# Optimization experiments

Hardware: AMD Instinct MI355X
Metric: run time of the kernel (lower is better)

The kernel has to match this reference:

```python
import jax, jax.numpy as jnp
import numpy as np

N = 100000      # nodes
E = 3200000     # edges (avg degree 32)
F_IN = 512      # num_features
H = 256         # hidden
C = 64          # num_classes
K = 20          # APPNP propagation steps
ALPHA = 0.1     # teleport probability


def setup_inputs() -> dict:
    key = jax.random.key(0)
    k0, k1, k2, k3 = jax.random.split(key, 4)
    x = jax.random.normal(k0, (N, F_IN), dtype=jnp.float32)
    edge_index = jax.random.randint(k1, (2, E), 0, N, dtype=jnp.int64)
    W1 = jax.random.normal(k2, (F_IN, H), dtype=jnp.float32) / np.sqrt(F_IN).astype(np.float32)
    b1 = jnp.zeros((H,), jnp.float32)
    W2 = jax.random.normal(k3, (H, C), dtype=jnp.float32) / np.sqrt(H).astype(np.float32)
    b2 = jnpp = jnp.zeros((C,), jnp.float32)
    return {"x": x, "edge_index": edge_index, "W1": W1, "b1": b1, "W2": W2, "b2": b2}


def reference(x, edge_index, W1, b1, W2, b2):
    n = x.shape[0]
    # MLP encoder (dropout is identity in eval mode)
    h = jax.nn.relu(x @ W1 + b1) @ W2 + b2            # [N, C]

    # gcn_norm with added self-loops (PyG APPNP default)
    self_loop = jnp.arange(n, dtype=edge_index.dtype)
    src = jnp.concatenate([edge_index[0], self_loop])  # message sources
    dst = jnp.concatenate([edge_index[1], self_loop])  # aggregation targets
    deg = jax.ops.segment_sum(jnp.ones_like(dst, jnp.float32), dst, num_segments=n)
    deg_inv_sqrt = jnp.where(deg > 0, jax.lax.rsqrt(deg), 0.0)
    norm = (deg_inv_sqrt[src] * deg_inv_sqrt[dst])[:, None]  # [E+N, 1]

    def prop_step(_, z):
        msg = z[src] * norm                               # gather + scale
        agg = jax.ops.segment_sum(msg, dst, num_segments=n)  # scatter-add
        return (1.0 - ALPHA) * agg + ALPHA * h            # teleport mix

    z = jax.lax.fori_loop(0, K, prop_step, h)
    return jax.nn.log_softmax(z, axis=1)
```

## Files before the change

### kernel.cpp

```cpp
#include <hip/hip_runtime.h>
#include <hip/hip_bf16.h>
#include <math.h>

#define NN 100000
#define EE 3200000
#define FIN 512
#define HID 256
#define CLS 64
#define KST 20

typedef __attribute__((ext_vector_type(8))) short bf16x8;
typedef __attribute__((ext_vector_type(4))) float f32x4;

__device__ __forceinline__ short f2bf(float f) {
    union { __hip_bfloat16 b; short s; } u;
    u.b = __float2bfloat16(f);
    return u.s;
}
__device__ __forceinline__ float bf2f(__hip_bfloat16 b) { return __bfloat162float(b); }


__global__ void zero_kernel(int* __restrict__ degcnt, int* __restrict__ cursor) {
    int i = blockIdx.x * 256 + threadIdx.x;
    if (i < NN) { degcnt[i] = 0; cursor[i] = 0; }
}

__global__ void count_kernel(const int* __restrict__ edst, int* __restrict__ degcnt) {
    int e = blockIdx.x * 256 + threadIdx.x;
    if (e < EE) atomicAdd(&degcnt[edst[e]], 1);
}

__global__ __launch_bounds__(1024) void scan1_kernel(const int* __restrict__ degcnt,
                                                     int* __restrict__ tmp,
                                                     int* __restrict__ bsum) {
    __shared__ int s[1024];
    int t = threadIdx.x;
    int i = blockIdx.x * 1024 + t;
    int v = (i < NN) ? degcnt[i] : 0;
    s[t] = v;
    __syncthreads();
    for (int off = 1; off < 1024; off <<= 1) {
        int xv = (t >= off) ? s[t - off] : 0;
        __syncthreads();
        s[t] += xv;
        __syncthreads();
    }
    if (i < NN) tmp[i] = s[t] - v;
    if (t == 1023) bsum[blockIdx.x] = s[1023];
}

__global__ void scan2_kernel(const int* __restrict__ bsum, int* __restrict__ boff, int nb) {
    if (blockIdx.x == 0 && threadIdx.x == 0) {
        int run = 0;
        for (int b = 0; b < nb; ++b) { boff[b] = run; run += bsum[b]; }
    }
}

__global__ void finalize_kernel(const int* __restrict__ tmp, const int* __restrict__ boff,
                                const int* __restrict__ degcnt,
                                int* __restrict__ rowptr, float* __restrict__ dis) {
    int i = blockIdx.x * 256 + threadIdx.x;
    if (i < NN) {
        rowptr[i] = tmp[i] + boff[i >> 10];
        dis[i] = rsqrtf((float)(degcnt[i] + 1));
        if (i == 0) rowptr[NN] = EE;
    }
}

__global__ void fill_kernel(const int* __restrict__ esrc, const int* __restrict__ edst,
                            const int* __restrict__ rowptr, int* __restrict__ cursor,
                            int* __restrict__ csrc) {
    int e = blockIdx.x * 256 + threadIdx.x;
    if (e < EE) {
        int d = edst[e];
        int pos = atomicAdd(&cursor[d], 1);
        csrc[rowptr[d] + pos] = esrc[e];
    }
}


__global__ void w1t_kernel(const float* __restrict__ W1, __hip_bfloat16* __restrict__ W1Tt) {
    const int c = threadIdx.x;
    const int kg = blockIdx.x;
    bf16x8 o;
#pragma unroll
    for (int j = 0; j < 8; ++j) o[j] = f2bf(W1[(size_t)(kg * 8 + j) * HID + c]);
    size_t dst = ((size_t)((c >> 4) * 16 + (kg >> 2))) * 512 + (c & 15) * 32 + (kg & 3) * 8;
    *(bf16x8*)((short*)W1Tt + dst) = o;
}

__global__ void w2t_kernel(const float* __restrict__ W2, __hip_bfloat16* __restrict__ W2Tt) {
    const int c = threadIdx.x;
    const int kg = blockIdx.x;
    bf16x8 o;
#pragma unroll
    for (int j = 0; j < 8; ++j) o[j] = f2bf(W2[(size_t)(kg * 8 + j) * CLS + c]);
    size_t dst = ((size_t)((c >> 4) * 8 + (kg >> 2))) * 512 + (c & 15) * 32 + (kg & 3) * 8;
    *(bf16x8*)((short*)W2Tt + dst) = o;
}

__device__ __forceinline__ bf16x8 load_a8(const float* p) {
    const float4 f0 = *(const float4*)p;
    const float4 f1 = *(const float4*)(p + 4);
    bf16x8 r;
    r[0] = f2bf(f0.x); r[1] = f2bf(f0.y); r[2] = f2bf(f0.z); r[3] = f2bf(f0.w);
    r[4] = f2bf(f1.x); r[5] = f2bf(f1.y); r[6] = f2bf(f1.z); r[7] = f2bf(f1.w);
    return r;
}

__global__ __launch_bounds__(256, 2) void mlp_kernel(const float* __restrict__ x,
                                                     const __hip_bfloat16* __restrict__ W1Tt,
                                                     const float* __restrict__ b1,
                                                     const __hip_bfloat16* __restrict__ W2Tt,
                                                     const float* __restrict__ b2,
                                                     const float* __restrict__ dis,
                                                     __hip_bfloat16* __restrict__ hb,
                                                     __hip_bfloat16* __restrict__ y0) {
    __shared__ __align__(16) char Tlds[64 * 512];

    const int t = threadIdx.x;
    const int w = t >> 6;
    const int lane = t & 63;
    const int lg = lane >> 4;
    const int li = lane & 15;
    const int loff = li * 32 + lg * 8;
    const int r0 = blockIdx.x * 64;

    const short* W1s = (const short*)W1Tt;
    const short* W2s = (const short*)W2Tt;

    const float* xrow[4];
#pragma unroll
    for (int mf = 0; mf < 4; ++mf) {
        int r = r0 + mf * 16 + li;
        xrow[mf] = x + (size_t)((r < NN) ? r : (NN - 1)) * FIN;
    }

    f32x4 acc1[4][4];
#pragma unroll
    for (int mf = 0; mf < 4; ++mf)
#pragma unroll
        for (int nf = 0; nf < 4; ++nf)
#pragma unroll
            for (int r = 0; r < 4; ++r) acc1[mf][nf][r] = 0.f;

#pragma unroll
    for (int kt = 0; kt < 16; ++kt) {
        bf16x8 bfw[4];
#pragma unroll
        for (int nf = 0; nf < 4; ++nf)
            bfw[nf] = *(const bf16x8*)(W1s + ((size_t)((w * 4 + nf) * 16 + kt)) * 512 + loff);
#pragma unroll
        for (int mf = 0; mf < 4; ++mf) {
            bf16x8 af = load_a8(xrow[mf] + kt * 32 + lg * 8);
#pragma unroll
            for (int nf = 0; nf < 4; ++nf)
                acc1[mf][nf] = __builtin_amdgcn_mfma_f32_16x16x32_bf16(
                    af, bfw[nf], acc1[mf][nf], 0, 0, 0);
        }
    }

#pragma unroll
    for (int nf = 0; nf < 4; ++nf) {
        const float bv = b1[w * 64 + nf * 16 + li];
        const int col = w * 64 + nf * 16 + li;
#pragma unroll
        for (int mf = 0; mf < 4; ++mf) {
#pragma unroll
            for (int r = 0; r < 4; ++r) {
                int row = mf * 16 + lg * 4 + r;
                float tv = fmaxf(acc1[mf][nf][r] + bv, 0.f);
                int byte = row * 512 + ((col * 2) ^ ((row & 7) << 4));
                *(short*)(Tlds + byte) = f2bf(tv);
            }
        }
    }
    __syncthreads();

    f32x4 acc2[4];
#pragma unroll
    for (int nf = 0; nf < 4; ++nf)
#pragma unroll
        for (int r = 0; r < 4; ++r) acc2[nf][r] = 0.f;

#pragma unroll
    for (int kt2 = 0; kt2 < 8; ++kt2) {
        int row = w * 16 + li;
        int kb = (kt2 * 32 + lg * 8) * 2;
        bf16x8 at = *(const bf16x8*)(Tlds + row * 512 + (kb ^ ((row & 7) << 4)));
#pragma unroll
        for (int nf = 0; nf < 4; ++nf) {
            bf16x8 bw = *(const bf16x8*)(W2s + ((size_t)(nf * 8 + kt2)) * 512 + loff);
            acc2[nf] = __builtin_amdgcn_mfma_f32_16x16x32_bf16(at, bw, acc2[nf], 0, 0, 0);
        }
    }

#pragma unroll
    for (int r = 0; r < 4; ++r) {
        int row = r0 + w * 16 + lg * 4 + r;
        if (row < NN) {
            const float dv = dis[row];
#pragma unroll
            for (int nf = 0; nf < 4; ++nf) {
                float hv = acc2[nf][r] + b2[nf * 16 + li];
                size_t o = (size_t)row * CLS + nf * 16 + li;
                hb[o] = __float2bfloat16(hv);
                y0[o] = __float2bfloat16(hv * dv);
            }
        }
    }
}

template <int LAST>
__global__ __launch_bounds__(256) void prop_kernel(const __hip_bfloat16* __restrict__ yin,
                                                   const __hip_bfloat16* __restrict__ hb,
                                                   const float* __restrict__ dis,
                                                   const int* __restrict__ rowptr,
                                                   const int* __restrict__ csrc,
                                                   __hip_bfloat16* __restrict__ yout,
                                                   float* __restrict__ zout) {
    const int node = blockIdx.x * 4 + (threadIdx.x >> 6);
    const int lane = threadIdx.x & 63;

    int p = __builtin_amdgcn_readfirstlane(rowptr[node]);
    const int e = __builtin_amdgcn_readfirstlane(rowptr[node + 1]);

    const __hip_bfloat16* Y = yin + lane;

    float a0 = bf2f(Y[(size_t)node << 6]);
    float a1 = 0.f, a2 = 0.f, a3 = 0.f;

    for (; p + 16 <= e; p += 16) {
        const int4 i0 = *(const int4*)(csrc + p);
        const int4 i1 = *(const int4*)(csrc + p + 4);
        const int4 i2 = *(const int4*)(csrc + p + 8);
        const int4 i3 = *(const int4*)(csrc + p + 12);
        float v0 = bf2f(Y[(size_t)i0.x << 6]);
        float v1 = bf2f(Y[(size_t)i0.y << 6]);
        float v2 = bf2f(Y[(size_t)i0.z << 6]);
        float v3 = bf2f(Y[(size_t)i0.w << 6]);
        float v4 = bf2f(Y[(size_t)i1.x << 6]);
        float v5 = bf2f(Y[(size_t)i1.y << 6]);
        float v6 = bf2f(Y[(size_t)i1.z << 6]);
        float v7 = bf2f(Y[(size_t)i1.w << 6]);
        float v8 = bf2f(Y[(size_t)i2.x << 6]);
        float v9 = bf2f(Y[(size_t)i2.y << 6]);
        float va = bf2f(Y[(size_t)i2.z << 6]);
        float vb = bf2f(Y[(size_t)i2.w << 6]);
        float vc = bf2f(Y[(size_t)i3.x << 6]);
        float vd = bf2f(Y[(size_t)i3.y << 6]);
        float ve = bf2f(Y[(size_t)i3.z << 6]);
        float vf = bf2f(Y[(size_t)i3.w << 6]);
        a0 += (v0 + v1) + (v2 + v3);
        a1 += (v4 + v5) + (v6 + v7);
        a2 += (v8 + v9) + (va + vb);
        a3 += (vc + vd) + (ve + vf);
    }
    for (; p + 4 <= e; p += 4) {
        const int4 i0 = *(const int4*)(csrc + p);
        float v0 = bf2f(Y[(size_t)i0.x << 6]);
        float v1 = bf2f(Y[(size_t)i0.y << 6]);
        float v2 = bf2f(Y[(size_t)i0.z << 6]);
        float v3 = bf2f(Y[(size_t)i0.w << 6]);
        a1 += (v0 + v1) + (v2 + v3);
    }
    for (; p < e; ++p)
        a2 += bf2f(Y[(size_t)csrc[p] << 6]);

    const float acc = (a0 + a1) + (a2 + a3);
    const float din = dis[node];
    const float z = 0.9f * din * acc + 0.1f * bf2f(hb[((size_t)node << 6) + lane]);

    if (LAST) {
        float m = z;
#pragma unroll
        for (int o = 32; o; o >>= 1) m = fmaxf(m, __shfl_xor(m, o));
        float ev = __expf(z - m);
        float s = ev;
#pragma unroll
        for (int o = 32; o; o >>= 1) s += __shfl_xor(s, o);
        zout[((size_t)node << 6) + lane] = z - m - __logf(s);
    } else {
        yout[((size_t)node << 6) + lane] = __float2bfloat16(z * din);
    }
}

extern "C" void kernel_launch(void* const* d_in, const int* in_sizes, int n_in,
                              void* d_out, int out_size, void* d_ws, size_t ws_size,
                              hipStream_t stream) {
    const float* x  = (const float*)d_in[0];
    const int*   ei = (const int*)d_in[1];
    const float* W1 = (const float*)d_in[2];
    const float* b1 = (const float*)d_in[3];
    const float* W2 = (const float*)d_in[4];
    const float* b2 = (const float*)d_in[5];
    float* out = (float*)d_out;

    const int* esrc = ei;
    const int* edst = ei + EE;

    char* w = (char*)d_ws;
    auto alloc = [&](size_t bytes) {
        char* p = w;
        w += (bytes + 255) & ~(size_t)255;
        return p;
    };
    __hip_bfloat16* hb   = (__hip_bfloat16*)alloc((size_t)NN * CLS * 2);
    __hip_bfloat16* y0   = (__hip_bfloat16*)alloc((size_t)NN * CLS * 2);
    __hip_bfloat16* y1   = (__hip_bfloat16*)alloc((size_t)NN * CLS * 2);
    __hip_bfloat16* W1Tt = (__hip_bfloat16*)alloc((size_t)HID * FIN * 2);
    __hip_bfloat16* W2Tt = (__hip_bfloat16*)alloc((size_t)CLS * HID * 2);
    float* dis   = (float*)alloc((size_t)NN * 4);
    int* degcnt  = (int*)alloc((size_t)NN * 4);
    int* tmp     = (int*)alloc((size_t)NN * 4);
    int* rowptr  = (int*)alloc((size_t)(NN + 1) * 4);
    int* cursor  = (int*)alloc((size_t)NN * 4);
    int* csrc    = (int*)alloc((size_t)EE * 4);
    int* bsum    = (int*)alloc(128 * 4);
    int* boff    = (int*)alloc(128 * 4);

    const int nbN = (NN + 255) / 256;
    const int nbE = (EE + 255) / 256;
    const int nscan = (NN + 1023) / 1024;

    zero_kernel<<<nbN, 256, 0, stream>>>(degcnt, cursor);
    count_kernel<<<nbE, 256, 0, stream>>>(edst, degcnt);
    scan1_kernel<<<nscan, 1024, 0, stream>>>(degcnt, tmp, bsum);
    scan2_kernel<<<1, 64, 0, stream>>>(bsum, boff, nscan);
    finalize_kernel<<<nbN, 256, 0, stream>>>(tmp, boff, degcnt, rowptr, dis);
    fill_kernel<<<nbE, 256, 0, stream>>>(esrc, edst, rowptr, cursor, csrc);

    w1t_kernel<<<FIN / 8, HID, 0, stream>>>(W1, W1Tt);
    w2t_kernel<<<HID / 8, CLS, 0, stream>>>(W2, W2Tt);

    mlp_kernel<<<(NN + 63) / 64, 256, 0, stream>>>(x, W1Tt, b1, W2Tt, b2, dis, hb, y0);

    const __hip_bfloat16* yin = y0;
    __hip_bfloat16* yout = y1;
    for (int s = 0; s < KST - 1; ++s) {
        prop_kernel<0><<<NN / 4, 256, 0, stream>>>(yin, hb, dis, rowptr, csrc, yout, nullptr);
        const __hip_bfloat16* t2 = yin;
        yin = yout;
        yout = (__hip_bfloat16*)t2;
    }
    prop_kernel<1><<<NN / 4, 256, 0, stream>>>(yin, hb, dis, rowptr, csrc, nullptr, out);
}
```

Before: 1.629 ms.

## Split propagation features into column blocks and stage MLP input through LDS

Node features are stored in four 16-column blocks, each NN×16 bf16, so each propagation pass works on a 3.2 MB slice that is more likely to stay in L2/MALL during random gathers. Each wave handles one node with four edge slots times 16 columns and reduces across slots with shuffles, and a separate log-softmax kernel reassembles the blocks. The MLP now stages x through swizzled LDS with coalesced prefetch and targets 3 blocks per CU. The cost is four times as many edge-index reads and launched waves per step, plus an extra fp32 z buffer and an extra kernel.

```diff
diff --git a/kernel.cpp b/kernel.cpp
--- a/kernel.cpp
+++ b/kernel.cpp
@@ -8,6 +8,7 @@
 #define HID 256
 #define CLS 64
 #define KST 20
+#define NBLK 25000
 
 typedef __attribute__((ext_vector_type(8))) short bf16x8;
 typedef __attribute__((ext_vector_type(4))) float f32x4;
@@ -18,6 +19,11 @@
     return u.s;
 }
 __device__ __forceinline__ float bf2f(__hip_bfloat16 b) { return __bfloat162float(b); }
+__device__ __forceinline__ float bfbits2f(short s) {
+    union { float f; unsigned u; } x;
+    x.u = ((unsigned)(unsigned short)s) << 16;
+    return x.f;
+}
 
 
 __global__ void zero_kernel(int* __restrict__ degcnt, int* __restrict__ cursor) {
@@ -99,23 +105,15 @@
     *(bf16x8*)((short*)W2Tt + dst) = o;
 }
 
-__device__ __forceinline__ bf16x8 load_a8(const float* p) {
-    const float4 f0 = *(const float4*)p;
-    const float4 f1 = *(const float4*)(p + 4);
-    bf16x8 r;
-    r[0] = f2bf(f0.x); r[1] = f2bf(f0.y); r[2] = f2bf(f0.z); r[3] = f2bf(f0.w);
-    r[4] = f2bf(f1.x); r[5] = f2bf(f1.y); r[6] = f2bf(f1.z); r[7] = f2bf(f1.w);
-    return r;
-}
-
-__global__ __launch_bounds__(256, 2) void mlp_kernel(const float* __restrict__ x,
+__global__ __launch_bounds__(256, 3) void mlp_kernel(const float* __restrict__ x,
                                                      const __hip_bfloat16* __restrict__ W1Tt,
                                                      const float* __restrict__ b1,
                                                      const __hip_bfloat16* __restrict__ W2Tt,
                                                      const float* __restrict__ b2,
                                                      const float* __restrict__ dis,
-                                                     __hip_bfloat16* __restrict__ hb,
+                                                     __hip_bfloat16* __restrict__ hbk,
                                                      __hip_bfloat16* __restrict__ y0) {
+    __shared__ __align__(16) char Alds[64 * 256];
     __shared__ __align__(16) char Tlds[64 * 512];
 
     const int t = threadIdx.x;
@@ -129,12 +127,20 @@
     const short* W1s = (const short*)W1Tt;
     const short* W2s = (const short*)W2Tt;
 
-    const float* xrow[4];
-#pragma unroll
-    for (int mf = 0; mf < 4; ++mf) {
-        int r = r0 + mf * 16 + li;
-        xrow[mf] = x + (size_t)((r < NN) ? r : (NN - 1)) * FIN;
-    }
+    const float* xp[8];
+    int srow[8], sc4[8];
+#pragma unroll
+    for (int i = 0; i < 8; ++i) {
+        int f = t + i * 256;
+        srow[i] = f >> 5;
+        sc4[i] = (f & 31) << 2;
+        int sr = r0 + srow[i]; if (sr >= NN) sr = NN - 1;
+        xp[i] = x + (size_t)sr * FIN + sc4[i];
+    }
+
+    float4 av[8];
+#pragma unroll
+    for (int i = 0; i < 8; ++i) av[i] = *(const float4*)(xp[i]);
 
     f32x4 acc1[4][4];
 #pragma unroll
@@ -144,20 +150,45 @@
 #pragma unroll
             for (int r = 0; r < 4; ++r) acc1[mf][nf][r] = 0.f;
 
-#pragma unroll
-    for (int kt = 0; kt < 16; ++kt) {
-        bf16x8 bfw[4];
-#pragma unroll
-        for (int nf = 0; nf < 4; ++nf)
-            bfw[nf] = *(const bf16x8*)(W1s + ((size_t)((w * 4 + nf) * 16 + kt)) * 512 + loff);
-#pragma unroll
-        for (int mf = 0; mf < 4; ++mf) {
-            bf16x8 af = load_a8(xrow[mf] + kt * 32 + lg * 8);
+    for (int kc = 0; kc < 4; ++kc) {
+#pragma unroll
+        for (int i = 0; i < 8; ++i) {
+            short4 b;
+            b.x = f2bf(av[i].x); b.y = f2bf(av[i].y); b.z = f2bf(av[i].z); b.w = f2bf(av[i].w);
+            int byte = srow[i] * 256 + ((sc4[i] * 2) ^ ((srow[i] & 7) << 4));
+            *(short4*)(Alds + byte) = b;
+        }
+        asm volatile("s_waitcnt lgkmcnt(0)" ::: "memory");
+        __builtin_amdgcn_s_barrier();
+        asm volatile("" ::: "memory");
+
+        if (kc < 3) {
+#pragma unroll
+            for (int i = 0; i < 8; ++i) av[i] = *(const float4*)(xp[i] + (kc + 1) * 128);
+        }
+
+#pragma unroll
+        for (int ks = 0; ks < 4; ++ks) {
+            bf16x8 af[4], bfw[4];
+#pragma unroll
+            for (int mf = 0; mf < 4; ++mf) {
+                int row = mf * 16 + li;
+                int kb = (ks * 32 + lg * 8) * 2;
+                af[mf] = *(const bf16x8*)(Alds + row * 256 + (kb ^ ((row & 7) << 4)));
+            }
 #pragma unroll
             for (int nf = 0; nf < 4; ++nf)
-                acc1[mf][nf] = __builtin_amdgcn_mfma_f32_16x16x32_bf16(
-                    af, bfw[nf], acc1[mf][nf], 0, 0, 0);
-        }
+                bfw[nf] = *(const bf16x8*)(W1s + ((size_t)((w * 4 + nf) * 16 + kc * 4 + ks)) * 512 + loff);
+#pragma unroll
+            for (int mf = 0; mf < 4; ++mf)
+#pragma unroll
+                for (int nf = 0; nf < 4; ++nf)
+                    acc1[mf][nf] = __builtin_amdgcn_mfma_f32_16x16x32_bf16(
+                        af[mf], bfw[nf], acc1[mf][nf], 0, 0, 0);
+        }
+        asm volatile("" ::: "memory");
+        __builtin_amdgcn_s_barrier();
+        asm volatile("" ::: "memory");
     }
 
 #pragma unroll
@@ -203,8 +234,8 @@
 #pragma unroll
             for (int nf = 0; nf < 4; ++nf) {
                 float hv = acc2[nf][r] + b2[nf * 16 + li];
-                size_t o = (size_t)row * CLS + nf * 16 + li;
-                hb[o] = __float2bfloat16(hv);
+                size_t o = (size_t)nf * (NN * 16) + (size_t)row * 16 + li;
+                hbk[o] = __float2bfloat16(hv);
                 y0[o] = __float2bfloat16(hv * dv);
             }
         }
@@ -212,77 +243,78 @@
 }
 
 template <int LAST>
-__global__ __launch_bounds__(256) void prop_kernel(const __hip_bfloat16* __restrict__ yin,
-                                                   const __hip_bfloat16* __restrict__ hb,
-                                                   const float* __restrict__ dis,
-                                                   const int* __restrict__ rowptr,
-                                                   const int* __restrict__ csrc,
-                                                   __hip_bfloat16* __restrict__ yout,
-                                                   float* __restrict__ zout) {
+__global__ __launch_bounds__(256) void prop_blk(const __hip_bfloat16* __restrict__ yin,
+                                                const __hip_bfloat16* __restrict__ hbk,
+                                                const float* __restrict__ dis,
+                                                const int* __restrict__ rowptr,
+                                                const int* __restrict__ csrc,
+                                                __hip_bfloat16* __restrict__ yout,
+                                                float* __restrict__ zout) {
+    const int pass = blockIdx.y;
     const int node = blockIdx.x * 4 + (threadIdx.x >> 6);
     const int lane = threadIdx.x & 63;
+    const int slot = lane >> 4;
+    const int c = lane & 15;
+
+    const short* Y = (const short*)yin + (size_t)pass * (NN * 16);
 
     int p = __builtin_amdgcn_readfirstlane(rowptr[node]);
     const int e = __builtin_amdgcn_readfirstlane(rowptr[node + 1]);
 
-    const __hip_bfloat16* Y = yin + lane;
-
-    float a0 = bf2f(Y[(size_t)node << 6]);
-    float a1 = 0.f, a2 = 0.f, a3 = 0.f;
-
+    const float self = bfbits2f(Y[node * 16 + c]);
+
+    float a0 = 0.f, a1 = 0.f, a2 = 0.f, a3 = 0.f;
     for (; p + 16 <= e; p += 16) {
-        const int4 i0 = *(const int4*)(csrc + p);
-        const int4 i1 = *(const int4*)(csrc + p + 4);
-        const int4 i2 = *(const int4*)(csrc + p + 8);
-        const int4 i3 = *(const int4*)(csrc + p + 12);
-        float v0 = bf2f(Y[(size_t)i0.x << 6]);
-        float v1 = bf2f(Y[(size_t)i0.y << 6]);
-        float v2 = bf2f(Y[(size_t)i0.z << 6]);
-        float v3 = bf2f(Y[(size_t)i0.w << 6]);
-        float v4 = bf2f(Y[(size_t)i1.x << 6]);
-        float v5 = bf2f(Y[(size_t)i1.y << 6]);
-        float v6 = bf2f(Y[(size_t)i1.z << 6]);
-        float v7 = bf2f(Y[(size_t)i1.w << 6]);
-        float v8 = bf2f(Y[(size_t)i2.x << 6]);
-        float v9 = bf2f(Y[(size_t)i2.y << 6]);
-        float va = bf2f(Y[(size_t)i2.z << 6]);
-        float vb = bf2f(Y[(size_t)i2.w << 6]);
-        float vc = bf2f(Y[(size_t)i3.x << 6]);
-        float vd = bf2f(Y[(size_t)i3.y << 6]);
-        float ve = bf2f(Y[(size_t)i3.z << 6]);
-        float vf = bf2f(Y[(size_t)i3.w << 6]);
-        a0 += (v0 + v1) + (v2 + v3);
-        a1 += (v4 + v5) + (v6 + v7);
-        a2 += (v8 + v9) + (va + vb);
-        a3 += (vc + vd) + (ve + vf);
+        int s0 = __builtin_nontemporal_load(csrc + p + slot);
+        int s1 = __builtin_nontemporal_load(csrc + p + 4 + slot);
+        int s2 = __builtin_nontemporal_load(csrc + p + 8 + slot);
+        int s3 = __builtin_nontemporal_load(csrc + p + 12 + slot);
+        a0 += bfbits2f(Y[s0 * 16 + c]);
+        a1 += bfbits2f(Y[s1 * 16 + c]);
+        a2 += bfbits2f(Y[s2 * 16 + c]);
+        a3 += bfbits2f(Y[s3 * 16 + c]);
     }
     for (; p + 4 <= e; p += 4) {
-        const int4 i0 = *(const int4*)(csrc + p);
-        float v0 = bf2f(Y[(size_t)i0.x << 6]);
-        float v1 = bf2f(Y[(size_t)i0.y << 6]);
-        float v2 = bf2f(Y[(size_t)i0.z << 6]);
-        float v3 = bf2f(Y[(size_t)i0.w << 6]);
-        a1 += (v0 + v1) + (v2 + v3);
-    }
-    for (; p < e; ++p)
-        a2 += bf2f(Y[(size_t)csrc[p] << 6]);
-
-    const float acc = (a0 + a1) + (a2 + a3);
+        int s = __builtin_nontemporal_load(csrc + p + slot);
+        a0 += bfbits2f(Y[s * 16 + c]);
+    }
+    if (p + slot < e) {
+        int s = __builtin_nontemporal_load(csrc + p + slot);
+        a1 += bfbits2f(Y[s * 16 + c]);
+    }
+
+    float acc = (a0 + a1) + (a2 + a3);
+    acc += __shfl_xor(acc, 16);
+    acc += __shfl_xor(acc, 32);
+    acc += self;
+
     const float din = dis[node];
-    const float z = 0.9f * din * acc + 0.1f * bf2f(hb[((size_t)node << 6) + lane]);
-
-    if (LAST) {
-        float m = z;
-#pragma unroll
-        for (int o = 32; o; o >>= 1) m = fmaxf(m, __shfl_xor(m, o));
-        float ev = __expf(z - m);
-        float s = ev;
-#pragma unroll
-        for (int o = 32; o; o >>= 1) s += __shfl_xor(s, o);
-        zout[((size_t)node << 6) + lane] = z - m - __logf(s);
-    } else {
-        yout[((size_t)node << 6) + lane] = __float2bfloat16(z * din);
-    }
+    const size_t o = (size_t)pass * (NN * 16) + (size_t)node * 16 + c;
+    const float z = 0.9f * din * acc + 0.1f * bf2f(hbk[o]);
+
+    if (slot == 0) {
+        if (LAST) {
+            __builtin_nontemporal_store(z, zout + o);
+        } else {
+            short v = f2bf(z * din);
+            __builtin_nontemporal_store(v, (short*)yout + o);
+        }
+    }
+}
+
+__global__ __launch_bounds__(256) void lsm_kernel(const float* __restrict__ zblk,
+                                                  float* __restrict__ out) {
+    const int node = blockIdx.x * 4 + (threadIdx.x >> 6);
+    const int lane = threadIdx.x & 63;
+    float z = zblk[(size_t)(lane >> 4) * (NN * 16) + (size_t)node * 16 + (lane & 15)];
+    float m = z;
+#pragma unroll
+    for (int o = 32; o; o >>= 1) m = fmaxf(m, __shfl_xor(m, o));
+    float ev = __expf(z - m);
+    float s = ev;
+#pragma unroll
+    for (int o = 32; o; o >>= 1) s += __shfl_xor(s, o);
+    out[(size_t)node * CLS + lane] = z - m - __logf(s);
 }
 
 extern "C" void kernel_launch(void* const* d_in, const int* in_sizes, int n_in,
@@ -305,9 +337,10 @@
         w += (bytes + 255) & ~(size_t)255;
         return p;
     };
-    __hip_bfloat16* hb   = (__hip_bfloat16*)alloc((size_t)NN * CLS * 2);
-    __hip_bfloat16* y0   = (__hip_bfloat16*)alloc((size_t)NN * CLS * 2);
-    __hip_bfloat16* y1   = (__hip_bfloat16*)alloc((size_t)NN * CLS * 2);
+    __hip_bfloat16* hbk  = (__hip_bfloat16*)alloc((size_t)NN * CLS * 2);
+    __hip_bfloat16* yA   = (__hip_bfloat16*)alloc((size_t)NN * CLS * 2);
+    __hip_bfloat16* yB   = (__hip_bfloat16*)alloc((size_t)NN * CLS * 2);
+    float*          zblk = (float*)alloc((size_t)NN * CLS * 4);
     __hip_bfloat16* W1Tt = (__hip_bfloat16*)alloc((size_t)HID * FIN * 2);
     __hip_bfloat16* W2Tt = (__hip_bfloat16*)alloc((size_t)CLS * HID * 2);
     float* dis   = (float*)alloc((size_t)NN * 4);
@@ -333,15 +366,17 @@
     w1t_kernel<<<FIN / 8, HID, 0, stream>>>(W1, W1Tt);
     w2t_kernel<<<HID / 8, CLS, 0, stream>>>(W2, W2Tt);
 
-    mlp_kernel<<<(NN + 63) / 64, 256, 0, stream>>>(x, W1Tt, b1, W2Tt, b2, dis, hb, y0);
-
-    const __hip_bfloat16* yin = y0;
-    __hip_bfloat16* yout = y1;
+    mlp_kernel<<<(NN + 63) / 64, 256, 0, stream>>>(x, W1Tt, b1, W2Tt, b2, dis, hbk, yA);
+
+    const __hip_bfloat16* yin = yA;
+    __hip_bfloat16* yout = yB;
     for (int s = 0; s < KST - 1; ++s) {
-        prop_kernel<0><<<NN / 4, 256, 0, stream>>>(yin, hb, dis, rowptr, csrc, yout, nullptr);
+        prop_blk<0><<<dim3(NBLK, 4), 256, 0, stream>>>(yin, hbk, dis, rowptr, csrc, yout, nullptr);
         const __hip_bfloat16* t2 = yin;
         yin = yout;
         yout = (__hip_bfloat16*)t2;
     }
-    prop_kernel<1><<<NN / 4, 256, 0, stream>>>(yin, hb, dis, rowptr, csrc, nullptr, out);
-}
+    prop_blk<1><<<dim3(NBLK, 4), 256, 0, stream>>>(yin, hbk, dis, rowptr, csrc, nullptr, zblk);
+
+    lsm_kernel<<<NBLK, 256, 0, stream>>>(zblk, out);
+}
```

Measured after the change: 4.767 ms. 193% more time.
